# Performance work log

Hardware: AMD Instinct MI355X
Metric: run time of the kernel (lower is better)

The kernel has to match this reference:

```python
import jax, jax.numpy as jnp
import numpy as np

B, C, L = 8192, 1, 4096
SCALES = 5
OUT_DIM = 512
STD_FACTOR = 1.0
SQRT_HALF = 0.7071067811865476  # Haar filter coefficient 1/sqrt(2)


def setup_inputs() -> dict:
    key = jax.random.key(0)
    k1, k2 = jax.random.split(key)
    x = jax.random.normal(k1, (B, C, L), dtype=jnp.float32)
    # kaiming_uniform_(a=0): bound = sqrt(2) * sqrt(3 / fan_in)
    fan_in = L  # in_dim_wave == in_dim for dyadic Haar
    bound = np.sqrt(2.0) * np.sqrt(3.0 / fan_in)
    block_mat = jax.random.uniform(k2, (L, OUT_DIM), dtype=jnp.float32,
                                   minval=-bound, maxval=bound)
    return {"x": x, "block_mat": block_mat}


def haar_analysis(x, scales):
    """Multi-level Haar DWT over last axis. Returns [cA_n, cD_n, ..., cD_1]."""
    details = []
    cur = x
    for _ in range(scales):
        even, odd = cur[..., ::2], cur[..., 1::2]
        details.append((even - odd) * SQRT_HALF)  # highpass
        cur = (even + odd) * SQRT_HALF            # lowpass
    return [cur] + details[::-1]


def reference(x, block_mat):
    coeffs = haar_analysis(x, SCALES)
    x_freq_cat = jnp.concatenate(coeffs, axis=-1)        # [B, C, L]
    c_no = x_freq_cat.shape[-1]
    x_freq_mat = x_freq_cat.reshape(-1, c_no)            # [B*C, L]
    a = jnp.abs(x_freq_mat)
    # torch.std is unbiased (ddof=1)
    threshold = jnp.mean(a) + jnp.std(a, ddof=1) * STD_FACTOR
    mask = a > threshold
    # sparse.mm(sparse(masked x), W) == (x * mask) @ W
    x_sparse = jnp.where(mask, x_freq_mat, jnp.zeros((), x_freq_mat.dtype))
    out = jax.nn.relu(x_sparse @ block_mat)              # [B*C, OUT_DIM]
    return out.reshape(x_freq_cat.shape[:-1] + (OUT_DIM,))
```

## Files before the change

### kernel.cpp

```cpp
#include <hip/hip_runtime.h>
#include <hip/hip_bf16.h>
#include <math.h>

#define LDIM 4096
#define NROWS 8192
#define NOUT 512

static const float SQRT_HALF_F = 0.70710678118654752440f;

typedef __attribute__((ext_vector_type(8))) short short8;
typedef __attribute__((ext_vector_type(4))) float f32x4;
typedef __attribute__((ext_vector_type(8))) unsigned short u16x8;
typedef __attribute__((ext_vector_type(4))) unsigned short u16x4;
typedef __attribute__((ext_vector_type(2))) unsigned short u16x2;

#define AM_OFF   0ull
#define WT_OFF   67108864ull
#define PART_OFF (WT_OFF + 4194304ull)
#define THR_OFF  (PART_OFF + 131072ull)

__device__ inline unsigned short f2bf(float f) {
  union { float f; unsigned u; } v; v.f = f;
  unsigned r = (v.u + 0x7fffu + ((v.u >> 16) & 1u)) >> 16;
  return (unsigned short)r;
}

__device__ inline unsigned short mcvt(float f, float thr) {
  return f2bf((fabsf(f) > thr) ? f : 0.0f);
}

__device__ inline void async16(void* l, const void* g) {
  __builtin_amdgcn_global_load_lds((const __attribute__((address_space(1))) void*)g,
                                   (__attribute__((address_space(3))) void*)l, 16, 0, 0);
}

__global__ __launch_bounds__(256) void haar1_kernel(const float* __restrict__ x,
                                                    double* __restrict__ partials,
                                                    const float* __restrict__ W,
                                                    unsigned short* __restrict__ Wt) {
  if (blockIdx.x >= NROWS) {
    __shared__ float tile[32][33];
    const int wb = blockIdx.x - NROWS;
    const int bx = wb & 15;
    const int by = wb >> 4;
    const int tx = threadIdx.x & 31, ty = threadIdx.x >> 5;
#pragma unroll
    for (int j = 0; j < 4; ++j)
      tile[ty + j * 8][tx] = W[(size_t)(by * 32 + ty + j * 8) * NOUT + bx * 32 + tx];
    __syncthreads();
#pragma unroll
    for (int j = 0; j < 4; ++j)
      Wt[(size_t)(bx * 32 + ty + j * 8) * LDIM + by * 32 + tx] = f2bf(tile[tx][ty + j * 8]);
    return;
  }

  __shared__ double red[8];
  const int row = blockIdx.x;
  const int t = threadIdx.x;
  const float S = SQRT_HALF_F;

  const float4* xr = (const float4*)(x + (size_t)row * LDIM) + 4 * t;
  float v[16];
#pragma unroll
  for (int k = 0; k < 4; ++k) {
    float4 q = xr[k];
    v[4 * k] = q.x; v[4 * k + 1] = q.y; v[4 * k + 2] = q.z; v[4 * k + 3] = q.w;
  }

  double sa = 0.0, sq = 0.0;
  float a1[8], a2[4], a3[2], a4;
#pragma unroll
  for (int j = 0; j < 8; ++j) {
    float d = (v[2 * j] - v[2 * j + 1]) * S;
    a1[j] = (v[2 * j] + v[2 * j + 1]) * S;
    sa += (double)fabsf(d); sq += (double)d * (double)d;
  }
#pragma unroll
  for (int j = 0; j < 4; ++j) {
    float d = (a1[2 * j] - a1[2 * j + 1]) * S;
    a2[j] = (a1[2 * j] + a1[2 * j + 1]) * S;
    sa += (double)fabsf(d); sq += (double)d * (double)d;
  }
#pragma unroll
  for (int j = 0; j < 2; ++j) {
    float d = (a2[2 * j] - a2[2 * j + 1]) * S;
    a3[j] = (a2[2 * j] + a2[2 * j + 1]) * S;
    sa += (double)fabsf(d); sq += (double)d * (double)d;
  }
  {
    float d = (a3[0] - a3[1]) * S;
    a4 = (a3[0] + a3[1]) * S;
    sa += (double)fabsf(d); sq += (double)d * (double)d;
  }
  {
    float other = __shfl_xor(a4, 1, 64);
    if ((t & 1) == 0) {
      float d = (a4 - other) * S, ap = (a4 + other) * S;
      sa += (double)fabsf(d) + (double)fabsf(ap);
      sq += (double)d * (double)d + (double)ap * (double)ap;
    }
  }

  const int lane = t & 63, wid = t >> 6;
#pragma unroll
  for (int off = 32; off > 0; off >>= 1) {
    sa += __shfl_down(sa, off, 64);
    sq += __shfl_down(sq, off, 64);
  }
  if (lane == 0) { red[wid] = sa; red[4 + wid] = sq; }
  __syncthreads();
  if (t == 0) {
    partials[2 * (size_t)row + 0] = red[0] + red[1] + red[2] + red[3];
    partials[2 * (size_t)row + 1] = red[4] + red[5] + red[6] + red[7];
  }
}

__global__ __launch_bounds__(1024) void thr_kernel(const double* __restrict__ partials,
                                                   float* __restrict__ thr) {
  __shared__ double red[32];
  const int tid = threadIdx.x;
  double sa = 0.0, sq = 0.0;
#pragma unroll
  for (int k = 0; k < NROWS / 1024; ++k) {
    int i = tid + k * 1024;
    sa += partials[2 * i + 0];
    sq += partials[2 * i + 1];
  }
  const int lane = tid & 63, wid = tid >> 6;
#pragma unroll
  for (int off = 32; off > 0; off >>= 1) {
    sa += __shfl_down(sa, off, 64);
    sq += __shfl_down(sq, off, 64);
  }
  if (lane == 0) { red[wid] = sa; red[16 + wid] = sq; }
  __syncthreads();
  if (tid == 0) {
    double s = 0.0, q = 0.0;
#pragma unroll
    for (int i = 0; i < 16; ++i) { s += red[i]; q += red[16 + i]; }
    const double n = (double)NROWS * (double)LDIM;
    double mean = s / n;
    double var = (q - s * s / n) / (n - 1.0);
    *thr = (float)(mean + sqrt(var));
  }
}

__global__ __launch_bounds__(256) void haar2_kernel(const float* __restrict__ x,
                                                    const float* __restrict__ thrp,
                                                    unsigned short* __restrict__ Am) {
  const float thr = *thrp;
  const int row = blockIdx.x;
  const int t = threadIdx.x;
  const float S = SQRT_HALF_F;

  const float4* xr = (const float4*)(x + (size_t)row * LDIM) + 4 * t;
  float v[16];
#pragma unroll
  for (int k = 0; k < 4; ++k) {
    float4 q = xr[k];
    v[4 * k] = q.x; v[4 * k + 1] = q.y; v[4 * k + 2] = q.z; v[4 * k + 3] = q.w;
  }

  unsigned short* orow = Am + (size_t)row * LDIM;
  float a1[8], a2[4], a3[2], a4;

  u16x8 d1;
#pragma unroll
  for (int j = 0; j < 8; ++j) {
    float d = (v[2 * j] - v[2 * j + 1]) * S;
    a1[j] = (v[2 * j] + v[2 * j + 1]) * S;
    d1[j] = mcvt(d, thr);
  }
  *(u16x8*)(orow + 2048 + 8 * t) = d1;

  u16x4 d2;
#pragma unroll
  for (int j = 0; j < 4; ++j) {
    float d = (a1[2 * j] - a1[2 * j + 1]) * S;
    a2[j] = (a1[2 * j] + a1[2 * j + 1]) * S;
    d2[j] = mcvt(d, thr);
  }
  *(u16x4*)(orow + 1024 + 4 * t) = d2;

  u16x2 d3;
#pragma unroll
  for (int j = 0; j < 2; ++j) {
    float d = (a2[2 * j] - a2[2 * j + 1]) * S;
    a3[j] = (a2[2 * j] + a2[2 * j + 1]) * S;
    d3[j] = mcvt(d, thr);
  }
  *(u16x2*)(orow + 512 + 2 * t) = d3;

  {
    float d = (a3[0] - a3[1]) * S;
    a4 = (a3[0] + a3[1]) * S;
    orow[256 + t] = mcvt(d, thr);
  }
  {
    float other = __shfl_xor(a4, 1, 64);
    if ((t & 1) == 0) {
      float d = (a4 - other) * S, ap = (a4 + other) * S;
      orow[128 + t / 2] = mcvt(d, thr);
      orow[t / 2] = mcvt(ap, thr);
    }
  }
}

#define GEMM_COMPUTE(ASB, BSB)                                                        \
  {                                                                                   \
    short8 af[2][2], bf[2][2];                                                        \
    _Pragma("unroll")                                                                 \
    for (int mi = 0; mi < 2; ++mi) {                                                  \
      const int arow = wm * 32 + mi * 16 + l15;                                       \
      _Pragma("unroll")                                                               \
      for (int ks = 0; ks < 2; ++ks)                                                  \
        af[mi][ks] = *(const short8*)&(ASB)[arow * 64 + ((ks * 4 + quad) ^ (arow & 7)) * 8]; \
    }                                                                                 \
    _Pragma("unroll")                                                                 \
    for (int ni = 0; ni < 2; ++ni) {                                                  \
      const int brow = wn * 32 + ni * 16 + l15;                                       \
      _Pragma("unroll")                                                               \
      for (int ks = 0; ks < 2; ++ks)                                                  \
        bf[ni][ks] = *(const short8*)&(BSB)[brow * 64 + ((ks * 4 + quad) ^ (brow & 7)) * 8]; \
    }                                                                                 \
    _Pragma("unroll")                                                                 \
    for (int ks = 0; ks < 2; ++ks)                                                    \
      _Pragma("unroll")                                                               \
      for (int mi = 0; mi < 2; ++mi)                                                  \
        _Pragma("unroll")                                                             \
        for (int ni = 0; ni < 2; ++ni)                                                \
          acc[mi][ni] = __builtin_amdgcn_mfma_f32_16x16x32_bf16(af[mi][ks], bf[ni][ks], \
                                                                acc[mi][ni], 0, 0, 0); \
  }

__global__ __launch_bounds__(512) void gemm_kernel(const unsigned short* __restrict__ Am,
                                                   const unsigned short* __restrict__ Wt,
                                                   float* __restrict__ out) {
  __shared__ __align__(16) unsigned short As[2][128 * 64];
  __shared__ __align__(16) unsigned short Bs[2][64 * 64];

  const int tid = threadIdx.x;
  const int lane = tid & 63, w = tid >> 6;
  const int quad = lane >> 4, l15 = lane & 15;
  const int wm = w >> 1, wn = w & 1;

  const int id = blockIdx.x;
  const int xcd = id & 7, slot = id >> 3;
  const int nblk = slot & 7;
  const int mblk = (slot >> 3) * 8 + xcd;
  const int n0 = nblk * 64, m0 = mblk * 128;

  f32x4 acc[2][2] = {};

  const int rl = lane >> 3;
  const int cg = (lane & 7) ^ rl;
  const unsigned short* AgBase = Am + (size_t)(m0 + rl) * LDIM + cg * 8;
  const unsigned short* BgBase = Wt + (size_t)(n0 + rl) * LDIM + cg * 8;

#define GEMM_STAGE(buf, k0)                                                            \
  {                                                                                    \
    _Pragma("unroll")                                                                  \
    for (int j = 0; j < 2; ++j)                                                        \
      async16(&As[buf][(w * 2 + j) * 512], AgBase + (size_t)((w * 2 + j) * 8) * LDIM + (k0)); \
    async16(&Bs[buf][w * 512], BgBase + (size_t)(w * 8) * LDIM + (k0));                \
  }

  GEMM_STAGE(0, 0);
  asm volatile("s_waitcnt vmcnt(0)" ::: "memory");
  __builtin_amdgcn_s_barrier();
  __builtin_amdgcn_sched_barrier(0);

  int cur = 0;
  for (int t = 0; t < (LDIM / 64) - 1; ++t) {
    GEMM_STAGE(cur ^ 1, (t + 1) * 64);
    GEMM_COMPUTE(As[cur], Bs[cur]);
    asm volatile("s_waitcnt vmcnt(0)" ::: "memory");
    __builtin_amdgcn_s_barrier();
    __builtin_amdgcn_sched_barrier(0);
    cur ^= 1;
  }
  GEMM_COMPUTE(As[cur], Bs[cur]);

#pragma unroll
  for (int mi = 0; mi < 2; ++mi) {
#pragma unroll
    for (int ni = 0; ni < 2; ++ni) {
      const int r0 = m0 + wm * 32 + mi * 16 + quad * 4;
      const int c = n0 + wn * 32 + ni * 16 + l15;
#pragma unroll
      for (int r = 0; r < 4; ++r)
        out[(size_t)(r0 + r) * NOUT + c] = fmaxf(acc[mi][ni][r], 0.0f);
    }
  }
}

extern "C" void kernel_launch(void* const* d_in, const int* in_sizes, int n_in,
                              void* d_out, int out_size, void* d_ws, size_t ws_size,
                              hipStream_t stream) {
  const float* x = (const float*)d_in[0];
  const float* W = (const float*)d_in[1];
  float* out = (float*)d_out;

  char* ws = (char*)d_ws;
  unsigned short* Am = (unsigned short*)(ws + AM_OFF);
  unsigned short* Wt = (unsigned short*)(ws + WT_OFF);
  double* partials = (double*)(ws + PART_OFF);
  float* thr = (float*)(ws + THR_OFF);

  haar1_kernel<<<NROWS + 2048, 256, 0, stream>>>(x, partials, W, Wt);
  thr_kernel<<<1, 1024, 0, stream>>>(partials, thr);
  haar2_kernel<<<NROWS, 256, 0, stream>>>(x, thr, Am);
  gemm_kernel<<<512, 512, 0, stream>>>(Am, Wt, out);
}
```

Before: 266.4 us.

## Switch GEMM to 32x32 MFMA with split-K across waves and triple buffering

Reorganizes the bf16 GEMM so each wave computes a 64x64 output tile with 32x32x16 MFMA instructions over a quarter of each 64-wide K slice, and the four K-partial accumulators are reduced through shared memory at the end. The LDS pipeline goes from double to triple buffering with partial vmcnt waits, so loads for two stages ahead can be in flight. The aim is larger MFMA tiles with more reuse per fragment load and better latency hiding. The cost is a serialized shared-memory reduction epilogue, more LDS use (lower occupancy), and more accumulator registers.

Result: no change. 270.1 us (+1.4%).

```diff
diff --git a/kernel.cpp b/kernel.cpp
--- a/kernel.cpp
+++ b/kernel.cpp
@@ -10,6 +10,7 @@
 
 typedef __attribute__((ext_vector_type(8))) short short8;
 typedef __attribute__((ext_vector_type(4))) float f32x4;
+typedef __attribute__((ext_vector_type(16))) float f32x16;
 typedef __attribute__((ext_vector_type(8))) unsigned short u16x8;
 typedef __attribute__((ext_vector_type(4))) unsigned short u16x4;
 typedef __attribute__((ext_vector_type(2))) unsigned short u16x2;
@@ -206,43 +207,17 @@
   }
 }
 
-#define GEMM_COMPUTE(ASB, BSB)                                                        \
-  {                                                                                   \
-    short8 af[2][2], bf[2][2];                                                        \
-    _Pragma("unroll")                                                                 \
-    for (int mi = 0; mi < 2; ++mi) {                                                  \
-      const int arow = wm * 32 + mi * 16 + l15;                                       \
-      _Pragma("unroll")                                                               \
-      for (int ks = 0; ks < 2; ++ks)                                                  \
-        af[mi][ks] = *(const short8*)&(ASB)[arow * 64 + ((ks * 4 + quad) ^ (arow & 7)) * 8]; \
-    }                                                                                 \
-    _Pragma("unroll")                                                                 \
-    for (int ni = 0; ni < 2; ++ni) {                                                  \
-      const int brow = wn * 32 + ni * 16 + l15;                                       \
-      _Pragma("unroll")                                                               \
-      for (int ks = 0; ks < 2; ++ks)                                                  \
-        bf[ni][ks] = *(const short8*)&(BSB)[brow * 64 + ((ks * 4 + quad) ^ (brow & 7)) * 8]; \
-    }                                                                                 \
-    _Pragma("unroll")                                                                 \
-    for (int ks = 0; ks < 2; ++ks)                                                    \
-      _Pragma("unroll")                                                               \
-      for (int mi = 0; mi < 2; ++mi)                                                  \
-        _Pragma("unroll")                                                             \
-        for (int ni = 0; ni < 2; ++ni)                                                \
-          acc[mi][ni] = __builtin_amdgcn_mfma_f32_16x16x32_bf16(af[mi][ks], bf[ni][ks], \
-                                                                acc[mi][ni], 0, 0, 0); \
-  }
-
 __global__ __launch_bounds__(512) void gemm_kernel(const unsigned short* __restrict__ Am,
                                                    const unsigned short* __restrict__ Wt,
                                                    float* __restrict__ out) {
-  __shared__ __align__(16) unsigned short As[2][128 * 64];
-  __shared__ __align__(16) unsigned short Bs[2][64 * 64];
+  __shared__ __align__(16) unsigned short As[3][128 * 64];
+  __shared__ __align__(16) unsigned short Bs[3][64 * 64];
 
   const int tid = threadIdx.x;
   const int lane = tid & 63, w = tid >> 6;
-  const int quad = lane >> 4, l15 = lane & 15;
-  const int wm = w >> 1, wn = w & 1;
+  const int l31 = lane & 31, hi = lane >> 5;
+  const int tm = w >> 2;
+  const int ws = w & 3;
 
   const int id = blockIdx.x;
   const int xcd = id & 7, slot = id >> 3;
@@ -250,7 +225,7 @@
   const int mblk = (slot >> 3) * 8 + xcd;
   const int n0 = nblk * 64, m0 = mblk * 128;
 
-  f32x4 acc[2][2] = {};
+  f32x16 acc[2][2] = {};
 
   const int rl = lane >> 3;
   const int cg = (lane & 7) ^ rl;
@@ -265,32 +240,99 @@
     async16(&Bs[buf][w * 512], BgBase + (size_t)(w * 8) * LDIM + (k0));                \
   }
 
+#define GEMM_COMPUTE(ASB, BSB)                                                        \
+  {                                                                                   \
+    short8 af[2], bfg[2];                                                             \
+    _Pragma("unroll")                                                                 \
+    for (int fi = 0; fi < 2; ++fi) {                                                  \
+      const int arow = tm * 64 + fi * 32 + l31;                                       \
+      af[fi] = *(const short8*)&(ASB)[arow * 64 + (((ws * 2 + hi) ^ (arow & 7)) * 8)]; \
+    }                                                                                 \
+    _Pragma("unroll")                                                                 \
+    for (int fj = 0; fj < 2; ++fj) {                                                  \
+      const int brow = fj * 32 + l31;                                                 \
+      bfg[fj] = *(const short8*)&(BSB)[brow * 64 + (((ws * 2 + hi) ^ (brow & 7)) * 8)]; \
+    }                                                                                 \
+    _Pragma("unroll")                                                                 \
+    for (int fi = 0; fi < 2; ++fi)                                                    \
+      _Pragma("unroll")                                                               \
+      for (int fj = 0; fj < 2; ++fj)                                                  \
+        acc[fi][fj] = __builtin_amdgcn_mfma_f32_32x32x16_bf16(af[fi], bfg[fj],        \
+                                                              acc[fi][fj], 0, 0, 0);  \
+  }
+
   GEMM_STAGE(0, 0);
+  GEMM_STAGE(1, 64);
+  asm volatile("s_waitcnt vmcnt(3)" ::: "memory");
+  __builtin_amdgcn_s_barrier();
+  __builtin_amdgcn_sched_barrier(0);
+
+  int ib0 = 0, ib1 = 1, ib2 = 2;
+  for (int t = 0; t < (LDIM / 64) - 2; ++t) {
+    GEMM_STAGE(ib2, (t + 2) * 64);
+    GEMM_COMPUTE(As[ib0], Bs[ib0]);
+    asm volatile("s_waitcnt vmcnt(3)" ::: "memory");
+    __builtin_amdgcn_s_barrier();
+    __builtin_amdgcn_sched_barrier(0);
+    const int tmp = ib0; ib0 = ib1; ib1 = ib2; ib2 = tmp;
+  }
+  GEMM_COMPUTE(As[ib0], Bs[ib0]);
   asm volatile("s_waitcnt vmcnt(0)" ::: "memory");
   __builtin_amdgcn_s_barrier();
   __builtin_amdgcn_sched_barrier(0);
-
-  int cur = 0;
-  for (int t = 0; t < (LDIM / 64) - 1; ++t) {
-    GEMM_STAGE(cur ^ 1, (t + 1) * 64);
-    GEMM_COMPUTE(As[cur], Bs[cur]);
-    asm volatile("s_waitcnt vmcnt(0)" ::: "memory");
-    __builtin_amdgcn_s_barrier();
-    __builtin_amdgcn_sched_barrier(0);
-    cur ^= 1;
-  }
-  GEMM_COMPUTE(As[cur], Bs[cur]);
-
-#pragma unroll
-  for (int mi = 0; mi < 2; ++mi) {
-#pragma unroll
-    for (int ni = 0; ni < 2; ++ni) {
-      const int r0 = m0 + wm * 32 + mi * 16 + quad * 4;
-      const int c = n0 + wn * 32 + ni * 16 + l15;
-#pragma unroll
-      for (int r = 0; r < 4; ++r)
-        out[(size_t)(r0 + r) * NOUT + c] = fmaxf(acc[mi][ni][r], 0.0f);
-    }
+  GEMM_COMPUTE(As[ib1], Bs[ib1]);
+  __syncthreads();
+
+  float* sc = (float*)&As[0][0];
+#define SC_WRITE()                                                                    \
+  { _Pragma("unroll")                                                                 \
+    for (int fi = 0; fi < 2; ++fi)                                                    \
+      _Pragma("unroll")                                                               \
+      for (int fj = 0; fj < 2; ++fj)                                                  \
+        _Pragma("unroll")                                                             \
+        for (int q = 0; q < 4; ++q) {                                                 \
+          f32x4 v;                                                                    \
+          v[0] = acc[fi][fj][4 * q + 0]; v[1] = acc[fi][fj][4 * q + 1];               \
+          v[2] = acc[fi][fj][4 * q + 2]; v[3] = acc[fi][fj][4 * q + 3];               \
+          *(f32x4*)&sc[tm * 4096 + (fi * 2 + fj) * 1024 + q * 256 + lane * 4] = v;    \
+        } }
+#define SC_ADD()                                                                      \
+  { _Pragma("unroll")                                                                 \
+    for (int fi = 0; fi < 2; ++fi)                                                    \
+      _Pragma("unroll")                                                               \
+      for (int fj = 0; fj < 2; ++fj)                                                  \
+        _Pragma("unroll")                                                             \
+        for (int q = 0; q < 4; ++q) {                                                 \
+          f32x4 v = *(const f32x4*)&sc[tm * 4096 + (fi * 2 + fj) * 1024 + q * 256 + lane * 4]; \
+          acc[fi][fj][4 * q + 0] += v[0]; acc[fi][fj][4 * q + 1] += v[1];             \
+          acc[fi][fj][4 * q + 2] += v[2]; acc[fi][fj][4 * q + 3] += v[3];             \
+        } }
+
+  if (ws == 1) SC_WRITE();
+  __syncthreads();
+  if (ws == 0) SC_ADD();
+  __syncthreads();
+  if (ws == 3) SC_WRITE();
+  __syncthreads();
+  if (ws == 2) SC_ADD();
+  __syncthreads();
+  if (ws == 2) SC_WRITE();
+  __syncthreads();
+  if (ws == 0) {
+    SC_ADD();
+#pragma unroll
+    for (int fi = 0; fi < 2; ++fi)
+#pragma unroll
+      for (int fj = 0; fj < 2; ++fj) {
+        const int c = n0 + fj * 32 + l31;
+#pragma unroll
+        for (int q = 0; q < 4; ++q)
+#pragma unroll
+          for (int j = 0; j < 4; ++j) {
+            const int r = m0 + tm * 64 + fi * 32 + 8 * q + 4 * hi + j;
+            out[(size_t)r * NOUT + c] = fmaxf(acc[fi][fj][4 * q + j], 0.0f);
+          }
+      }
   }
 }
 
```
